# Kernel tuning notes

Hardware: AMD Instinct MI355X
Metric: run time of the kernel (lower is better)

The kernel has to match this reference:

```python
import jax, jax.numpy as jnp
import numpy as np

FP4_E2M1_VALUES = jnp.array([0.0, 0.5, 1.0, 1.5, 2.0, 3.0, 4.0, 6.0,
                             -0.0, -0.5, -1.0, -1.5, -2.0, -3.0, -4.0, -6.0],
                            dtype=jnp.float32)

OUT_F, IN_F, BS = 4096, 4096, 16


def setup_inputs() -> dict:
    key = jax.random.key(0)
    k1, k2, k3, k4 = jax.random.split(key, 4)
    x = jax.random.normal(k1, (4, 2048, IN_F), dtype=jnp.float32)
    weight_indices = jax.random.randint(k2, (OUT_F, IN_F // BS, BS), 0, 16, dtype=jnp.int32)
    weight_scales = jax.random.uniform(k3, (OUT_F, IN_F // BS), dtype=jnp.float32)
    bias = jax.random.normal(k4, (OUT_F,), dtype=jnp.float32)
    return {"x": x, "weight_indices": weight_indices,
            "weight_scales": weight_scales, "bias": bias}


def reference(x, weight_indices, weight_scales, bias):
    # Dequantize: gather FP4 values per index, scale per block of 16.
    idx = jnp.clip(weight_indices, 0, 15)              # [O, NB, BS]
    vals = FP4_E2M1_VALUES[idx]                        # [O, NB, BS]
    weight = (vals * weight_scales[:, :, None]).reshape(OUT_F, IN_F)
    # F.linear: y = x @ W^T + b
    return jnp.einsum('bsi,oi->bso', x, weight) + bias
```

## Files before the change

kernel.cpp:

```cpp
#include <hip/hip_runtime.h>
#include <hip/hip_bf16.h>

static constexpr int M_TOT = 8192;
static constexpr int N_TOT = 4096;
static constexpr int K_TOT = 4096;

static constexpr int BM = 256, BN = 256, BK = 32;
static constexpr int NT = K_TOT / BK;
static constexpr int GTHREADS = 512;
static constexpr int BUF_BYTES = 32768;
static constexpr int LDS_BYTES = 4 * BUF_BYTES;

typedef __bf16 bf16x8 __attribute__((ext_vector_type(8)));
typedef float f32x4 __attribute__((ext_vector_type(4)));
typedef unsigned short u16x8 __attribute__((ext_vector_type(8)));
typedef const __attribute__((address_space(1))) f32x4* gf4p;

__device__ __forceinline__ unsigned short f2bf(float f) {
  return __builtin_bit_cast(unsigned short, (__bf16)f);
}

__device__ __forceinline__ float fp4_decode(int idx) {
  unsigned u = (unsigned)idx & 15u;
  unsigned sgn = (u >> 3) << 31;
  unsigned mag = u & 7u;
  unsigned e = mag >> 1, m = mag & 1u;
  unsigned bits = (e == 0u) ? (m ? 0x3F000000u : 0u)
                            : (((126u + e) << 23) | (m << 22));
  return __uint_as_float(bits | sgn);
}

__device__ __forceinline__ void glds16(const void* g, void* l) {
  __builtin_amdgcn_global_load_lds(
      (__attribute__((address_space(1))) void*)g,
      (__attribute__((address_space(3))) void*)l, 16, 0, 0);
}

__global__ __launch_bounds__(256) void dequant_w_kernel(
    const int* __restrict__ idx, const float* __restrict__ scales,
    unsigned short* __restrict__ W) {
  const int t = blockIdx.x * 256 + threadIdx.x;
  const int4 v = reinterpret_cast<const int4*>(idx)[t];
  const float s = scales[t >> 2];
  ushort4 o;
  o.x = f2bf(fp4_decode(v.x) * s);
  o.y = f2bf(fp4_decode(v.y) * s);
  o.z = f2bf(fp4_decode(v.z) * s);
  o.w = f2bf(fp4_decode(v.w) * s);
  reinterpret_cast<ushort4*>(W)[t] = o;
}

__global__ __launch_bounds__(GTHREADS, 1) void gemm256(
    const float* __restrict__ X, const unsigned short* __restrict__ B,
    const float* __restrict__ bias, float* __restrict__ out) {
  extern __shared__ char smem[];

  const int t = threadIdx.x;
  const int lane = t & 63, wid = t >> 6;
  const int wr = wid >> 2;
  const int wc = wid & 3;
  const int ln = lane & 15;
  const int kc = lane >> 4;

  const int bid = blockIdx.x;
  const int bmi = (bid & 7) * 4 + ((bid >> 3) & 3);
  const int bni = bid >> 5;
  const int bm0 = bmi * BM, bn0 = bni * BN;

  const int row_s = t >> 2;
  const int kcd = (t & 3) ^ ((t >> 3) & 3);
  const float* gxA = X + (size_t)(bm0 + row_s) * K_TOT + kcd * 8;
  const unsigned short* gB = B + (size_t)(bn0 + row_s) * K_TOT + kcd * 8;
  char* ldsB = smem + 16384 + t * 16;

  const int swz = (kc ^ ((ln >> 1) & 3)) * 16;
  const int base_a = (wr * 128 + ln) * 64 + swz;
  const int base_b = 16384 + (wc * 64 + ln) * 64 + swz;

  f32x4 acc[8][4];
#pragma unroll
  for (int i = 0; i < 8; ++i)
#pragma unroll
    for (int j = 0; j < 4; ++j) acc[i][j] = f32x4{0.f, 0.f, 0.f, 0.f};

  bf16x8 afA[4], afB[4], bfE[4], bfO[4];
  f32x4 ldE[4], ldO[4];

#define LD_A(dst, kt) do {                                              \
    const float* q_ = gxA + (size_t)(kt) * BK;                          \
    const float* r_ = q_ + (size_t)128 * K_TOT;                         \
    dst[0] = ((gf4p)(q_))[0];                                           \
    dst[1] = ((gf4p)(q_))[1];                                           \
    dst[2] = ((gf4p)(r_))[0];                                           \
    dst[3] = ((gf4p)(r_))[1];                                           \
  } while (0)

#define WR_A(src, bufi) do {                                            \
    u16x8 lo_, hi_;                                                     \
    lo_[0] = f2bf(src[0][0]); lo_[1] = f2bf(src[0][1]);                 \
    lo_[2] = f2bf(src[0][2]); lo_[3] = f2bf(src[0][3]);                 \
    lo_[4] = f2bf(src[1][0]); lo_[5] = f2bf(src[1][1]);                 \
    lo_[6] = f2bf(src[1][2]); lo_[7] = f2bf(src[1][3]);                 \
    hi_[0] = f2bf(src[2][0]); hi_[1] = f2bf(src[2][1]);                 \
    hi_[2] = f2bf(src[2][2]); hi_[3] = f2bf(src[2][3]);                 \
    hi_[4] = f2bf(src[3][0]); hi_[5] = f2bf(src[3][1]);                 \
    hi_[6] = f2bf(src[3][2]); hi_[7] = f2bf(src[3][3]);                 \
    *reinterpret_cast<u16x8*>(smem + (bufi) * BUF_BYTES + t * 16) = lo_; \
    *reinterpret_cast<u16x8*>(smem + (bufi) * BUF_BYTES + 8192 + t * 16) = hi_; \
  } while (0)

#define STAGE_B(kt, bufi) do {                                          \
    const unsigned short* s_ = gB + (size_t)(kt) * BK;                  \
    glds16(s_, ldsB + (bufi) * BUF_BYTES);                              \
    glds16(s_ + (size_t)128 * K_TOT, ldsB + (bufi) * BUF_BYTES + 8192); \
  } while (0)

#define READ_AF(dst, bufi, mb) do {                                     \
    const char* p_ = smem + (bufi) * BUF_BYTES + base_a + (mb) * 1024;  \
    dst[0] = *(const bf16x8*)(p_);                                      \
    dst[1] = *(const bf16x8*)(p_ + 1024);                               \
    dst[2] = *(const bf16x8*)(p_ + 2048);                               \
    dst[3] = *(const bf16x8*)(p_ + 3072);                               \
  } while (0)
#define READ_BF(dst, bufi) do {                                         \
    const char* p_ = smem + (bufi) * BUF_BYTES + base_b;                \
    dst[0] = *(const bf16x8*)(p_);                                      \
    dst[1] = *(const bf16x8*)(p_ + 1024);                               \
    dst[2] = *(const bf16x8*)(p_ + 2048);                               \
    dst[3] = *(const bf16x8*)(p_ + 3072);                               \
  } while (0)

#define MFMA16(afs, bfs, mb) do {                                       \
    __builtin_amdgcn_s_setprio(1);                                      \
    _Pragma("unroll")                                                   \
    for (int m_ = 0; m_ < 4; ++m_)                                      \
      _Pragma("unroll")                                                 \
      for (int n_ = 0; n_ < 4; ++n_)                                    \
        acc[(mb) + m_][n_] = __builtin_amdgcn_mfma_f32_16x16x32_bf16(   \
            afs[m_], bfs[n_], acc[(mb) + m_][n_], 0, 0, 0);             \
    __builtin_amdgcn_s_setprio(0);                                      \
  } while (0)

#define VM(n) asm volatile("s_waitcnt vmcnt(" #n ")" ::: "memory")
#define LGKM0 asm volatile("s_waitcnt lgkmcnt(0)" ::: "memory")
#define BAR __builtin_amdgcn_s_barrier()

#define PH_A(tt, rb, sb, bfc, ldN, ldW) do { \
    LD_A(ldN, (tt) + 4);       \
    READ_AF(afB, rb, 4);       \
    MFMA16(afA, bfc, 0);       \
    VM(6);                     \
    WR_A(ldW, sb);             \
    LGKM0; BAR;                \
  } while (0)
#define PH_B(tt, rbn, sb, bfc, bfn) do { \
    READ_AF(afA, rbn, 0);                \
    READ_BF(bfn, rbn);                   \
    STAGE_B((tt) + 3, sb);               \
    MFMA16(afB, bfc, 4);                 \
    BAR;                                 \
  } while (0)

  LD_A(ldE, 0); VM(0); WR_A(ldE, 0);
  LD_A(ldE, 1); VM(0); WR_A(ldE, 1);
  LD_A(ldE, 2); VM(0); WR_A(ldE, 2);
  STAGE_B(0, 0);
  asm volatile("" ::: "memory");
  STAGE_B(1, 1);
  asm volatile("" ::: "memory");
  STAGE_B(2, 2);
  LD_A(ldO, 3);
  VM(6);
  LGKM0;
  BAR;
  READ_AF(afA, 0, 0);
  READ_BF(bfE, 0);

#pragma unroll 1
  for (int tt = 0; tt < NT - 4; tt += 4) {
    PH_A(tt + 0, 0, 3, bfE, ldE, ldO);
    PH_B(tt + 0, 1, 3, bfE, bfO);
    PH_A(tt + 1, 1, 0, bfO, ldO, ldE);
    PH_B(tt + 1, 2, 0, bfO, bfE);
    PH_A(tt + 2, 2, 1, bfE, ldE, ldO);
    PH_B(tt + 2, 3, 1, bfE, bfO);
    PH_A(tt + 3, 3, 2, bfO, ldO, ldE);
    PH_B(tt + 3, 0, 2, bfO, bfE);
  }

  READ_AF(afB, 0, 4);
  MFMA16(afA, bfE, 0);
  VM(2);
  WR_A(ldO, 3);
  LGKM0; BAR;
  READ_AF(afA, 1, 0); READ_BF(bfO, 1); STAGE_B(127, 3); MFMA16(afB, bfE, 4); BAR;
  READ_AF(afB, 1, 4); MFMA16(afA, bfO, 0); VM(2); BAR;
  READ_AF(afA, 2, 0); READ_BF(bfE, 2); MFMA16(afB, bfO, 4); BAR;
  READ_AF(afB, 2, 4); MFMA16(afA, bfE, 0); VM(0); BAR;
  READ_AF(afA, 3, 0); READ_BF(bfO, 3); MFMA16(afB, bfE, 4); BAR;
  READ_AF(afB, 3, 4); MFMA16(afA, bfO, 0);
  MFMA16(afB, bfO, 4);

  const int orow0 = bm0 + wr * 128 + (lane >> 4) * 4;
  const int ocol0 = bn0 + wc * 64 + ln;
  float bj[4];
#pragma unroll
  for (int n = 0; n < 4; ++n) bj[n] = bias[ocol0 + n * 16];
#pragma unroll
  for (int mi = 0; mi < 8; ++mi)
#pragma unroll
    for (int n = 0; n < 4; ++n)
#pragma unroll
      for (int q = 0; q < 4; ++q)
        out[(size_t)(orow0 + mi * 16 + q) * N_TOT + ocol0 + n * 16] =
            acc[mi][n][q] + bj[n];
}

extern "C" void kernel_launch(void* const* d_in, const int* in_sizes, int n_in,
                              void* d_out, int out_size, void* d_ws, size_t ws_size,
                              hipStream_t stream) {
  const float* x = (const float*)d_in[0];
  const int* widx = (const int*)d_in[1];
  const float* wsc = (const float*)d_in[2];
  const float* bias = (const float*)d_in[3];
  float* out = (float*)d_out;

  unsigned short* Wbf = (unsigned short*)d_ws;

  dequant_w_kernel<<<dim3((N_TOT * (size_t)K_TOT / 4) / 256), dim3(256), 0, stream>>>(
      widx, wsc, Wbf);

  (void)hipFuncSetAttribute((const void*)gemm256,
                            hipFuncAttributeMaxDynamicSharedMemorySize, LDS_BYTES);
  gemm256<<<dim3((M_TOT / BM) * (N_TOT / BN)), dim3(GTHREADS), LDS_BYTES, stream>>>(
      x, Wbf, bias, out);
}
```

Measured before the change: 290.6 us.

## Reorder A-tile prefetch pipeline so global loads issue after LDS writes

Restructures the software pipeline for the A operand. Global loads for tile t+3 are now issued right after the register-held tile is written to LDS, instead of loading tile t+4 ahead, which shortens the prefetch distance by one stage. The prologue now preloads only tile 0 into LDS and keeps tiles 1 and 2 in flight in registers, and the epilogue is rewritten to drain the new schedule. The goal is better overlap of global loads with MFMA work and fewer vmcnt stalls. The shorter lead time may expose more memory latency.

```diff
diff --git a/kernel.cpp b/kernel.cpp
--- a/kernel.cpp
+++ b/kernel.cpp
@@ -145,60 +145,71 @@
 #define LGKM0 asm volatile("s_waitcnt lgkmcnt(0)" ::: "memory")
 #define BAR __builtin_amdgcn_s_barrier()
 
-#define PH_A(tt, rb, sb, bfc, ldN, ldW) do { \
-    LD_A(ldN, (tt) + 4);       \
-    READ_AF(afB, rb, 4);       \
-    MFMA16(afA, bfc, 0);       \
-    VM(6);                     \
-    WR_A(ldW, sb);             \
-    LGKM0; BAR;                \
-  } while (0)
-#define PH_B(tt, rbn, sb, bfc, bfn) do { \
-    READ_AF(afA, rbn, 0);                \
-    READ_BF(bfn, rbn);                   \
-    STAGE_B((tt) + 3, sb);               \
-    MFMA16(afB, bfc, 4);                 \
-    BAR;                                 \
+#define PH_A(tt_, rb, wb, bfc, ld) do { \
+    READ_AF(afB, rb, 4);                \
+    MFMA16(afA, bfc, 0);                \
+    VM(6);                              \
+    WR_A(ld, wb);                       \
+    LD_A(ld, (tt_) + 3);                \
+    LGKM0; BAR;                         \
+  } while (0)
+#define PH_B(tt_, rbn, sb, bfc, bfn) do { \
+    READ_AF(afA, rbn, 0);                 \
+    READ_BF(bfn, rbn);                    \
+    STAGE_B((tt_) + 3, sb);               \
+    MFMA16(afB, bfc, 4);                  \
+    BAR;                                  \
   } while (0)
 
   LD_A(ldE, 0); VM(0); WR_A(ldE, 0);
-  LD_A(ldE, 1); VM(0); WR_A(ldE, 1);
-  LD_A(ldE, 2); VM(0); WR_A(ldE, 2);
   STAGE_B(0, 0);
   asm volatile("" ::: "memory");
   STAGE_B(1, 1);
   asm volatile("" ::: "memory");
+  LD_A(ldO, 1);
+  asm volatile("" ::: "memory");
+  LD_A(ldE, 2);
+  asm volatile("" ::: "memory");
   STAGE_B(2, 2);
-  LD_A(ldO, 3);
-  VM(6);
+  VM(12);
   LGKM0;
   BAR;
   READ_AF(afA, 0, 0);
   READ_BF(bfE, 0);
 
 #pragma unroll 1
-  for (int tt = 0; tt < NT - 4; tt += 4) {
-    PH_A(tt + 0, 0, 3, bfE, ldE, ldO);
+  for (int tt = 0; tt < 124; tt += 4) {
+    PH_A(tt + 0, 0, 1, bfE, ldO);
     PH_B(tt + 0, 1, 3, bfE, bfO);
-    PH_A(tt + 1, 1, 0, bfO, ldO, ldE);
+    PH_A(tt + 1, 1, 2, bfO, ldE);
     PH_B(tt + 1, 2, 0, bfO, bfE);
-    PH_A(tt + 2, 2, 1, bfE, ldE, ldO);
+    PH_A(tt + 2, 2, 3, bfE, ldO);
     PH_B(tt + 2, 3, 1, bfE, bfO);
-    PH_A(tt + 3, 3, 2, bfO, ldO, ldE);
+    PH_A(tt + 3, 3, 0, bfO, ldE);
     PH_B(tt + 3, 0, 2, bfO, bfE);
   }
 
   READ_AF(afB, 0, 4);
   MFMA16(afA, bfE, 0);
-  VM(2);
+  VM(6);
+  WR_A(ldO, 1);
+  LD_A(ldO, 127);
+  LGKM0; BAR;
+  READ_AF(afA, 1, 0); READ_BF(bfO, 1); STAGE_B(127, 3); MFMA16(afB, bfE, 4); BAR;
+  READ_AF(afB, 1, 4);
+  MFMA16(afA, bfO, 0);
+  VM(6);
+  WR_A(ldE, 2);
+  LGKM0; BAR;
+  READ_AF(afA, 2, 0); READ_BF(bfE, 2); MFMA16(afB, bfO, 4); BAR;
+  READ_AF(afB, 2, 4);
+  MFMA16(afA, bfE, 0);
+  VM(0);
   WR_A(ldO, 3);
   LGKM0; BAR;
-  READ_AF(afA, 1, 0); READ_BF(bfO, 1); STAGE_B(127, 3); MFMA16(afB, bfE, 4); BAR;
-  READ_AF(afB, 1, 4); MFMA16(afA, bfO, 0); VM(2); BAR;
-  READ_AF(afA, 2, 0); READ_BF(bfE, 2); MFMA16(afB, bfO, 4); BAR;
-  READ_AF(afB, 2, 4); MFMA16(afA, bfE, 0); VM(0); BAR;
   READ_AF(afA, 3, 0); READ_BF(bfO, 3); MFMA16(afB, bfE, 4); BAR;
-  READ_AF(afB, 3, 4); MFMA16(afA, bfO, 0);
+  READ_AF(afB, 3, 4);
+  MFMA16(afA, bfO, 0);
   MFMA16(afB, bfO, 4);
 
   const int orow0 = bm0 + wr * 128 + (lane >> 4) * 4;
```

New measurement: 279.6 us. -3.8%, faster.
